# Optimization experiments

Hardware: AMD Instinct MI355X
Metric: run time of the kernel (lower is better)

## Reference

```python
import jax, jax.numpy as jnp
import numpy as np

EMBED = 512
HEADS = 8
HEAD_DIM = EMBED // HEADS
N, S = 4, 2048


def setup_inputs() -> dict:
    key = jax.random.key(0)
    ks = jax.random.split(key, 10)
    value = jax.random.normal(ks[0], (N, S, EMBED), dtype=jnp.float32)
    k_in = jax.random.normal(ks[1], (N, S, EMBED), dtype=jnp.float32)
    q_in = jax.random.normal(ks[2], (N, S, EMBED), dtype=jnp.float32)
    mask = jax.random.randint(ks[3], (N, 1, S, S), 0, 2, dtype=jnp.int32)
    s = 1.0 / np.sqrt(HEAD_DIM)
    Wq = jax.random.uniform(ks[4], (HEAD_DIM, HEAD_DIM), minval=-s, maxval=s, dtype=jnp.float32)
    Wk = jax.random.uniform(ks[5], (HEAD_DIM, HEAD_DIM), minval=-s, maxval=s, dtype=jnp.float32)
    Wv = jax.random.uniform(ks[6], (HEAD_DIM, HEAD_DIM), minval=-s, maxval=s, dtype=jnp.float32)
    so = 1.0 / np.sqrt(EMBED)
    Wo = jax.random.uniform(ks[7], (EMBED, EMBED), minval=-so, maxval=so, dtype=jnp.float32)
    bo = jax.random.uniform(ks[8], (EMBED,), minval=-so, maxval=so, dtype=jnp.float32)
    return {"value": value, "key": k_in, "query": q_in, "mask": mask,
            "Wq": Wq, "Wk": Wk, "Wv": Wv, "Wo": Wo, "bo": bo}


def reference(value, key, query, mask, Wq, Wk, Wv, Wo, bo):
    n, qlen = query.shape[0], query.shape[1]
    # split heads: (N, L, H, D)
    v = value.reshape(n, -1, HEADS, HEAD_DIM)
    k = key.reshape(n, -1, HEADS, HEAD_DIM)
    q = query.reshape(n, qlen, HEADS, HEAD_DIM)
    # per-head linear projections (torch Linear: x @ W^T, no bias)
    v = jnp.einsum('nlhd,ed->nlhe', v, Wv)
    k = jnp.einsum('nlhd,ed->nlhe', k, Wk)
    q = jnp.einsum('nqhd,ed->nqhe', q, Wq)
    # energy: (N, H, Q, K)
    energy = jnp.einsum('nqhd,nkhd->nhqk', q, k)
    energy = jnp.where(mask == 0, jnp.float32(-1e20), energy)
    # NOTE: original scales by sqrt(embed_size), not sqrt(head_dim)
    attn = jax.nn.softmax(energy / jnp.sqrt(jnp.float32(EMBED)), axis=3)
    out = jnp.einsum('nhql,nlhd->nqhd', attn, v).reshape(n, qlen, EMBED)
    return out @ Wo.T + bo
```

## Files before the change

### kernel.cpp

```cpp
#include <hip/hip_runtime.h>

typedef short short8 __attribute__((ext_vector_type(8)));
typedef float f32x4 __attribute__((ext_vector_type(4)));
typedef unsigned short ushort4v __attribute__((ext_vector_type(4)));
typedef unsigned long long u64;
typedef u64 u64x2 __attribute__((ext_vector_type(2)));

#define N_B   4
#define S_LEN 2048
#define EMB   512
#define HD    64
#define NHB   32
#define QSCALE 0.063758714f

#define EXP2F(x) __builtin_amdgcn_exp2f(x)

__device__ unsigned short g_Wqb[64*64];
__device__ unsigned short g_Wkb[64*64];
__device__ unsigned short g_Wvb[64*64];
__device__ unsigned short g_Wob[512*512];
__device__ unsigned short g_Qp[NHB*S_LEN*HD];
__device__ unsigned short g_Kp[NHB*S_LEN*HD];
__device__ unsigned short g_Vt[NHB*HD*S_LEN];
__device__ unsigned short g_AO[N_B*S_LEN*EMB];
__device__ u64            g_Mb[N_B*32*S_LEN];

__device__ __forceinline__ unsigned short f2bf(float f) {
  unsigned u = __float_as_uint(f);
  u = u + 0x7fffu + ((u >> 16) & 1u);
  return (unsigned short)(u >> 16);
}

__device__ __forceinline__ unsigned cvt_pk_bf16(float a, float b) {
  unsigned r;
  asm("v_cvt_pk_bf16_f32 %0, %1, %2" : "=v"(r) : "v"(a), "v"(b));
  return r;
}

__global__ __launch_bounds__(256) void k0_wconv(const float* __restrict__ Wq,
                                                const float* __restrict__ Wk,
                                                const float* __restrict__ Wv,
                                                const float* __restrict__ Wo) {
  int idx = blockIdx.x * 256 + threadIdx.x;
  if (idx < 4096)        g_Wqb[idx]         = f2bf(Wq[idx] * QSCALE);
  else if (idx < 8192)   g_Wkb[idx - 4096]  = f2bf(Wk[idx - 4096]);
  else if (idx < 12288)  g_Wvb[idx - 8192]  = f2bf(Wv[idx - 8192]);
  else                   g_Wob[idx - 12288] = f2bf(Wo[idx - 12288]);
}

__global__ __launch_bounds__(256) void k0b_mask(const int* __restrict__ mask) {
  int wid = blockIdx.x * 4 + (threadIdx.x >> 6);
  int lane = threadIdx.x & 63;
  int n = wid >> 11, q = wid & 2047;
  const int* base = mask + ((size_t)(n * 2048 + q) << 11);
  u64* dst = g_Mb + (size_t)n * 32 * S_LEN + q;
#pragma unroll 4
  for (int j = 0; j < 32; ++j) {
    int mk = base[j * 64 + lane];
    u64 bits = __ballot(mk != 0);
    if (lane == 0) dst[(size_t)j * S_LEN] = bits;
  }
}

__global__ __launch_bounds__(256) void k1_proj(const float* __restrict__ q_in,
                                               const float* __restrict__ k_in,
                                               const float* __restrict__ v_in) {
  __shared__ unsigned short VtL[64][72];
  const int tid = threadIdx.x;
  const int w = tid >> 6, lane = tid & 63, g = lane >> 4, c = lane & 15;
  const int s0 = blockIdx.x * 64;
  const int nh = blockIdx.y, n = nh >> 3, h = nh & 7;
  const int which = blockIdx.z;
  const float* src = which == 0 ? q_in : (which == 1 ? k_in : v_in);
  const unsigned short* Wb = which == 0 ? g_Wqb : (which == 1 ? g_Wkb : g_Wvb);

  short8 xb[2];
  const int srow = s0 + w * 16 + c;
#pragma unroll
  for (int ks = 0; ks < 2; ++ks) {
    const float* ap = src + ((size_t)n * S_LEN + srow) * EMB + h * HD + ks * 32 + g * 8;
    f32x4 x0 = *(const f32x4*)ap;
    f32x4 x1 = *(const f32x4*)(ap + 4);
    short8 tt;
    tt[0] = (short)f2bf(x0[0]); tt[1] = (short)f2bf(x0[1]);
    tt[2] = (short)f2bf(x0[2]); tt[3] = (short)f2bf(x0[3]);
    tt[4] = (short)f2bf(x1[0]); tt[5] = (short)f2bf(x1[1]);
    tt[6] = (short)f2bf(x1[2]); tt[7] = (short)f2bf(x1[3]);
    xb[ks] = tt;
  }

  f32x4 acc[4];
#pragma unroll
  for (int dt = 0; dt < 4; ++dt) { acc[dt][0]=0.f; acc[dt][1]=0.f; acc[dt][2]=0.f; acc[dt][3]=0.f; }

#pragma unroll
  for (int ks = 0; ks < 2; ++ks)
#pragma unroll
    for (int dt = 0; dt < 4; ++dt) {
      short8 a = *(const short8*)(Wb + (dt * 16 + c) * HD + ks * 32 + g * 8);
      acc[dt] = __builtin_amdgcn_mfma_f32_16x16x32_bf16(a, xb[ks], acc[dt], 0, 0, 0);
    }

  if (which < 2) {
    unsigned short* dst = which == 0 ? g_Qp : g_Kp;
#pragma unroll
    for (int dt = 0; dt < 4; ++dt) {
      ushort4v u;
      u[0] = f2bf(acc[dt][0]); u[1] = f2bf(acc[dt][1]);
      u[2] = f2bf(acc[dt][2]); u[3] = f2bf(acc[dt][3]);
      *(ushort4v*)(dst + ((size_t)nh * S_LEN + srow) * HD + dt * 16 + 4 * g) = u;
    }
  } else {
#pragma unroll
    for (int dt = 0; dt < 4; ++dt)
#pragma unroll
      for (int r = 0; r < 4; ++r)
        VtL[dt * 16 + 4 * g + r][w * 16 + c] = f2bf(acc[dt][r]);
    __syncthreads();
#pragma unroll
    for (int rep = 0; rep < 2; ++rep) {
      int cid = tid + rep * 256;
      int row = cid >> 3, ch = cid & 7;
      short8 v = *(const short8*)(&VtL[row][ch * 8]);
      *(short8*)(g_Vt + ((size_t)nh * HD + row) * S_LEN + s0 + ch * 8) = v;
    }
  }
}

__global__ __launch_bounds__(512) void k2_attn() {
  __shared__ unsigned short Kl[2][64][64];
  __shared__ unsigned short Vl[2][80][64];
  __shared__ unsigned short Pl[8][16][64];
  const int tid = threadIdx.x;
  const int w = tid >> 6, lane = tid & 63, g = lane >> 4, c = lane & 15;
  const int q0 = blockIdx.x * 128;
  const int nh = blockIdx.y, n = nh >> 3;

  short8 aq[2];
#pragma unroll
  for (int ks = 0; ks < 2; ++ks)
    aq[ks] = *(const short8*)(g_Qp + ((size_t)nh * S_LEN + q0 + w * 16 + c) * HD + ks * 32 + g * 8);

  const int strow = tid >> 3, schunk = tid & 7;
  const int sdst = (schunk ^ (strow & 7)) * 8;
  const unsigned short* ksrc = g_Kp + ((size_t)nh * S_LEN + strow) * HD + schunk * 8;
  const unsigned short* vsrc = g_Vt + ((size_t)nh * HD + strow) * S_LEN + schunk * 8;
  const u64* mbase = g_Mb + ((size_t)n * 32) * S_LEN + q0 + w * 16 + 4 * g;

  {
    int flat = tid * 4;
    int b = flat >> 10, rem = flat & 1023, rr = rem >> 6, cc = rem & 63;
    ushort4v ones4 = {0x3f80, 0x3f80, 0x3f80, 0x3f80};
    *(ushort4v*)(&Vl[b][64 + rr][cc]) = ones4;
  }

  f32x4 O4[4], O5;
#pragma unroll
  for (int dt = 0; dt < 4; ++dt) { O4[dt][0]=0.f; O4[dt][1]=0.f; O4[dt][2]=0.f; O4[dt][3]=0.f; }
  O5[0]=0.f; O5[1]=0.f; O5[2]=0.f; O5[3]=0.f;

  short8 kst = *(const short8*)(ksrc);
  short8 vst = *(const short8*)(vsrc);
  u64x2 mA = *(const u64x2*)(mbase);
  u64x2 mB = *(const u64x2*)(mbase + 2);
  *(short8*)(&Kl[0][strow][sdst]) = kst;
  *(short8*)(&Vl[0][strow][sdst]) = vst;
  __syncthreads();

  for (int t = 0; t < 32; ++t) {
    const int cur = t & 1;
    u64x2 mAn, mBn;
    if (t < 31) {
      kst = *(const short8*)(ksrc + (size_t)(t + 1) * 64 * HD);
      vst = *(const short8*)(vsrc + (t + 1) * 64);
      mAn = *(const u64x2*)(mbase + (size_t)(t + 1) * S_LEN);
      mBn = *(const u64x2*)(mbase + (size_t)(t + 1) * S_LEN + 2);
    }

    f32x4 sa[4];
#pragma unroll
    for (int ct = 0; ct < 4; ++ct) { sa[ct][0]=0.f; sa[ct][1]=0.f; sa[ct][2]=0.f; sa[ct][3]=0.f; }
#pragma unroll
    for (int ks = 0; ks < 2; ++ks)
#pragma unroll
      for (int ct = 0; ct < 4; ++ct) {
        short8 bk = *(const short8*)(&Kl[cur][ct * 16 + c][((g + 4 * ks) ^ (c & 7)) * 8]);
        sa[ct] = __builtin_amdgcn_mfma_f32_16x16x32_bf16(aq[ks], bk, sa[ct], 0, 0, 0);
      }

    unsigned lo0 = (unsigned)mA[0], hi0 = (unsigned)(mA[0] >> 32);
    unsigned lo1 = (unsigned)mA[1], hi1 = (unsigned)(mA[1] >> 32);
    unsigned lo2 = (unsigned)mB[0], hi2 = (unsigned)(mB[0] >> 32);
    unsigned lo3 = (unsigned)mB[1], hi3 = (unsigned)(mB[1] >> 32);
#pragma unroll
    for (int ct = 0; ct < 4; ++ct) {
      const int sh = (ct & 1) * 16 + c;
      float p0 = ((((ct & 2) ? hi0 : lo0) >> sh) & 1u) ? EXP2F(sa[ct][0]) : 0.f;
      float p1 = ((((ct & 2) ? hi1 : lo1) >> sh) & 1u) ? EXP2F(sa[ct][1]) : 0.f;
      float p2 = ((((ct & 2) ? hi2 : lo2) >> sh) & 1u) ? EXP2F(sa[ct][2]) : 0.f;
      float p3 = ((((ct & 2) ? hi3 : lo3) >> sh) & 1u) ? EXP2F(sa[ct][3]) : 0.f;
      unsigned pk01 = cvt_pk_bf16(p0, p1);
      unsigned pk23 = cvt_pk_bf16(p2, p3);
      const int col = ct * 16 + c;
      const int chs = ((col >> 3) << 3);
#pragma unroll
      for (int r = 0; r < 4; ++r) {
        int prow = 4 * g + r;
        unsigned pk = (r < 2) ? pk01 : pk23;
        unsigned short v = (r & 1) ? (unsigned short)(pk >> 16) : (unsigned short)pk;
        Pl[w][prow][(chs ^ ((prow & 7) << 3)) | (col & 7)] = v;
      }
    }

#pragma unroll
    for (int ks = 0; ks < 2; ++ks) {
      short8 pa = *(const short8*)(&Pl[w][c][((g + 4 * ks) ^ (c & 7)) * 8]);
#pragma unroll
      for (int dt = 0; dt < 5; ++dt) {
        short8 bv = *(const short8*)(&Vl[cur][dt * 16 + c][((g + 4 * ks) ^ (c & 7)) * 8]);
        if (dt < 4)
          O4[dt] = __builtin_amdgcn_mfma_f32_16x16x32_bf16(pa, bv, O4[dt], 0, 0, 0);
        else
          O5 = __builtin_amdgcn_mfma_f32_16x16x32_bf16(pa, bv, O5, 0, 0, 0);
      }
    }

    if (t < 31) {
      *(short8*)(&Kl[cur ^ 1][strow][sdst]) = kst;
      *(short8*)(&Vl[cur ^ 1][strow][sdst]) = vst;
      mA = mAn; mB = mBn;
      __syncthreads();
    }
  }

  const int h = nh & 7;
#pragma unroll
  for (int r = 0; r < 4; ++r) {
    float inv = O5[r] > 0.f ? 1.f / O5[r] : 0.f;
    int qr = q0 + w * 16 + 4 * g + r;
#pragma unroll
    for (int dt = 0; dt < 4; ++dt)
      g_AO[((size_t)n * S_LEN + qr) * EMB + h * HD + dt * 16 + c] = f2bf(O4[dt][r] * inv);
  }
}

__global__ __launch_bounds__(256) void k3_oproj(const float* __restrict__ bo,
                                                float* __restrict__ out) {
  const int tid = threadIdx.x;
  const int w = tid >> 6, lane = tid & 63, g = lane >> 4, c = lane & 15;
  const int m0 = blockIdx.x * 64;
  const int n0 = blockIdx.y * 64;

  f32x4 acc[4];
#pragma unroll
  for (int ct = 0; ct < 4; ++ct) { acc[ct][0]=0.f; acc[ct][1]=0.f; acc[ct][2]=0.f; acc[ct][3]=0.f; }

  for (int ks = 0; ks < 16; ++ks) {
    short8 a = *(const short8*)(g_AO + ((size_t)(m0 + w * 16 + c)) * EMB + ks * 32 + g * 8);
#pragma unroll
    for (int ct = 0; ct < 4; ++ct) {
      short8 b = *(const short8*)(g_Wob + (size_t)(n0 + ct * 16 + c) * EMB + ks * 32 + g * 8);
      acc[ct] = __builtin_amdgcn_mfma_f32_16x16x32_bf16(a, b, acc[ct], 0, 0, 0);
    }
  }

#pragma unroll
  for (int ct = 0; ct < 4; ++ct) {
    int col = n0 + ct * 16 + c;
    float bias = bo[col];
#pragma unroll
    for (int r = 0; r < 4; ++r) {
      int row = m0 + w * 16 + 4 * g + r;
      out[(size_t)row * EMB + col] = acc[ct][r] + bias;
    }
  }
}

extern "C" void kernel_launch(void* const* d_in, const int* in_sizes, int n_in,
                              void* d_out, int out_size, void* d_ws, size_t ws_size,
                              hipStream_t stream) {
  const float* value = (const float*)d_in[0];
  const float* key   = (const float*)d_in[1];
  const float* query = (const float*)d_in[2];
  const int*   mask  = (const int*)d_in[3];
  const float* Wq    = (const float*)d_in[4];
  const float* Wk    = (const float*)d_in[5];
  const float* Wv    = (const float*)d_in[6];
  const float* Wo    = (const float*)d_in[7];
  const float* bo    = (const float*)d_in[8];
  float* out = (float*)d_out;

  k0_wconv<<<1072, 256, 0, stream>>>(Wq, Wk, Wv, Wo);
  k0b_mask<<<2048, 256, 0, stream>>>(mask);
  k1_proj<<<dim3(32, 32, 3), 256, 0, stream>>>(query, key, value);
  k2_attn<<<dim3(16, 32), 512, 0, stream>>>();
  k3_oproj<<<dim3(128, 8), 256, 0, stream>>>(bo, out);
}
```

Measured before the change: 273.4 us.

## Merge prep kernels, loop heads in projection, remap attention block order

Folds the weight conversion and mask bit-packing into one kernel launch so there is one fewer launch. The projection kernel now loops over all 8 heads per block, loading the weight fragments once and reusing them, which cuts the grid from 3072 to 384 blocks. The attention grid is flattened to 1D with a custom mapping from block index to (head, query tile), likely to spread heads across XCDs or L2. Fewer projection blocks may underfill the GPU and serialize per-head work within each block.

```diff
diff --git a/kernel.cpp b/kernel.cpp
--- a/kernel.cpp
+++ b/kernel.cpp
@@ -3,6 +3,7 @@
 typedef short short8 __attribute__((ext_vector_type(8)));
 typedef float f32x4 __attribute__((ext_vector_type(4)));
 typedef unsigned short ushort4v __attribute__((ext_vector_type(4)));
+typedef unsigned int uint4v __attribute__((ext_vector_type(4)));
 typedef unsigned long long u64;
 typedef u64 u64x2 __attribute__((ext_vector_type(2)));
 
@@ -12,7 +13,6 @@
 #define HD    64
 #define NHB   32
 #define QSCALE 0.063758714f
-
 #define EXP2F(x) __builtin_amdgcn_exp2f(x)
 
 __device__ unsigned short g_Wqb[64*64];
@@ -30,35 +30,36 @@
   u = u + 0x7fffu + ((u >> 16) & 1u);
   return (unsigned short)(u >> 16);
 }
-
 __device__ __forceinline__ unsigned cvt_pk_bf16(float a, float b) {
   unsigned r;
   asm("v_cvt_pk_bf16_f32 %0, %1, %2" : "=v"(r) : "v"(a), "v"(b));
   return r;
 }
 
-__global__ __launch_bounds__(256) void k0_wconv(const float* __restrict__ Wq,
-                                                const float* __restrict__ Wk,
-                                                const float* __restrict__ Wv,
-                                                const float* __restrict__ Wo) {
-  int idx = blockIdx.x * 256 + threadIdx.x;
-  if (idx < 4096)        g_Wqb[idx]         = f2bf(Wq[idx] * QSCALE);
-  else if (idx < 8192)   g_Wkb[idx - 4096]  = f2bf(Wk[idx - 4096]);
-  else if (idx < 12288)  g_Wvb[idx - 8192]  = f2bf(Wv[idx - 8192]);
-  else                   g_Wob[idx - 12288] = f2bf(Wo[idx - 12288]);
-}
-
-__global__ __launch_bounds__(256) void k0b_mask(const int* __restrict__ mask) {
-  int wid = blockIdx.x * 4 + (threadIdx.x >> 6);
-  int lane = threadIdx.x & 63;
-  int n = wid >> 11, q = wid & 2047;
-  const int* base = mask + ((size_t)(n * 2048 + q) << 11);
-  u64* dst = g_Mb + (size_t)n * 32 * S_LEN + q;
+__global__ __launch_bounds__(256) void k0_prep(const float* __restrict__ Wq,
+                                               const float* __restrict__ Wk,
+                                               const float* __restrict__ Wv,
+                                               const float* __restrict__ Wo,
+                                               const int* __restrict__ mask) {
+  const int b = blockIdx.x;
+  if (b < 1072) {
+    int idx = b * 256 + threadIdx.x;
+    if (idx < 4096)        g_Wqb[idx]         = f2bf(Wq[idx] * QSCALE);
+    else if (idx < 8192)   g_Wkb[idx - 4096]  = f2bf(Wk[idx - 4096]);
+    else if (idx < 12288)  g_Wvb[idx - 8192]  = f2bf(Wv[idx - 8192]);
+    else                   g_Wob[idx - 12288] = f2bf(Wo[idx - 12288]);
+  } else {
+    int wid = (b - 1072) * 4 + (threadIdx.x >> 6);
+    int lane = threadIdx.x & 63;
+    int n = wid >> 11, q = wid & 2047;
+    const int* base = mask + ((size_t)(n * 2048 + q) << 11);
+    u64* dst = g_Mb + (size_t)n * 32 * S_LEN + q;
 #pragma unroll 4
-  for (int j = 0; j < 32; ++j) {
-    int mk = base[j * 64 + lane];
-    u64 bits = __ballot(mk != 0);
-    if (lane == 0) dst[(size_t)j * S_LEN] = bits;
+    for (int j = 0; j < 32; ++j) {
+      int mk = base[j * 64 + lane];
+      u64 bits = __ballot(mk != 0);
+      if (lane == 0) dst[(size_t)j * S_LEN] = bits;
+    }
   }
 }
 
@@ -69,60 +70,69 @@
   const int tid = threadIdx.x;
   const int w = tid >> 6, lane = tid & 63, g = lane >> 4, c = lane & 15;
   const int s0 = blockIdx.x * 64;
-  const int nh = blockIdx.y, n = nh >> 3, h = nh & 7;
+  const int n = blockIdx.y;
   const int which = blockIdx.z;
   const float* src = which == 0 ? q_in : (which == 1 ? k_in : v_in);
   const unsigned short* Wb = which == 0 ? g_Wqb : (which == 1 ? g_Wkb : g_Wvb);
 
-  short8 xb[2];
   const int srow = s0 + w * 16 + c;
-#pragma unroll
-  for (int ks = 0; ks < 2; ++ks) {
-    const float* ap = src + ((size_t)n * S_LEN + srow) * EMB + h * HD + ks * 32 + g * 8;
-    f32x4 x0 = *(const f32x4*)ap;
-    f32x4 x1 = *(const f32x4*)(ap + 4);
-    short8 tt;
-    tt[0] = (short)f2bf(x0[0]); tt[1] = (short)f2bf(x0[1]);
-    tt[2] = (short)f2bf(x0[2]); tt[3] = (short)f2bf(x0[3]);
-    tt[4] = (short)f2bf(x1[0]); tt[5] = (short)f2bf(x1[1]);
-    tt[6] = (short)f2bf(x1[2]); tt[7] = (short)f2bf(x1[3]);
-    xb[ks] = tt;
-  }
-
-  f32x4 acc[4];
-#pragma unroll
-  for (int dt = 0; dt < 4; ++dt) { acc[dt][0]=0.f; acc[dt][1]=0.f; acc[dt][2]=0.f; acc[dt][3]=0.f; }
-
+  const float* rowp = src + ((size_t)n * S_LEN + srow) * EMB;
+
+  short8 wf[2][4];
 #pragma unroll
   for (int ks = 0; ks < 2; ++ks)
 #pragma unroll
-    for (int dt = 0; dt < 4; ++dt) {
-      short8 a = *(const short8*)(Wb + (dt * 16 + c) * HD + ks * 32 + g * 8);
-      acc[dt] = __builtin_amdgcn_mfma_f32_16x16x32_bf16(a, xb[ks], acc[dt], 0, 0, 0);
-    }
-
-  if (which < 2) {
-    unsigned short* dst = which == 0 ? g_Qp : g_Kp;
-#pragma unroll
-    for (int dt = 0; dt < 4; ++dt) {
-      ushort4v u;
-      u[0] = f2bf(acc[dt][0]); u[1] = f2bf(acc[dt][1]);
-      u[2] = f2bf(acc[dt][2]); u[3] = f2bf(acc[dt][3]);
-      *(ushort4v*)(dst + ((size_t)nh * S_LEN + srow) * HD + dt * 16 + 4 * g) = u;
-    }
-  } else {
-#pragma unroll
     for (int dt = 0; dt < 4; ++dt)
-#pragma unroll
-      for (int r = 0; r < 4; ++r)
-        VtL[dt * 16 + 4 * g + r][w * 16 + c] = f2bf(acc[dt][r]);
-    __syncthreads();
-#pragma unroll
-    for (int rep = 0; rep < 2; ++rep) {
-      int cid = tid + rep * 256;
-      int row = cid >> 3, ch = cid & 7;
-      short8 v = *(const short8*)(&VtL[row][ch * 8]);
-      *(short8*)(g_Vt + ((size_t)nh * HD + row) * S_LEN + s0 + ch * 8) = v;
+      wf[ks][dt] = *(const short8*)(Wb + (dt * 16 + c) * HD + ks * 32 + g * 8);
+
+  for (int hd = 0; hd < 8; ++hd) {
+    short8 xb[2];
+#pragma unroll
+    for (int ks = 0; ks < 2; ++ks) {
+      const float* ap = rowp + hd * HD + ks * 32 + g * 8;
+      f32x4 x0 = *(const f32x4*)ap;
+      f32x4 x1 = *(const f32x4*)(ap + 4);
+      short8 tt;
+      tt[0] = (short)f2bf(x0[0]); tt[1] = (short)f2bf(x0[1]);
+      tt[2] = (short)f2bf(x0[2]); tt[3] = (short)f2bf(x0[3]);
+      tt[4] = (short)f2bf(x1[0]); tt[5] = (short)f2bf(x1[1]);
+      tt[6] = (short)f2bf(x1[2]); tt[7] = (short)f2bf(x1[3]);
+      xb[ks] = tt;
+    }
+    f32x4 acc[4];
+#pragma unroll
+    for (int dt = 0; dt < 4; ++dt) { acc[dt][0]=0.f; acc[dt][1]=0.f; acc[dt][2]=0.f; acc[dt][3]=0.f; }
+#pragma unroll
+    for (int ks = 0; ks < 2; ++ks)
+#pragma unroll
+      for (int dt = 0; dt < 4; ++dt)
+        acc[dt] = __builtin_amdgcn_mfma_f32_16x16x32_bf16(wf[ks][dt], xb[ks], acc[dt], 0, 0, 0);
+
+    const int nh = n * 8 + hd;
+    if (which < 2) {
+      unsigned short* dst = which == 0 ? g_Qp : g_Kp;
+#pragma unroll
+      for (int dt = 0; dt < 4; ++dt) {
+        ushort4v u;
+        u[0] = f2bf(acc[dt][0]); u[1] = f2bf(acc[dt][1]);
+        u[2] = f2bf(acc[dt][2]); u[3] = f2bf(acc[dt][3]);
+        *(ushort4v*)(dst + ((size_t)nh * S_LEN + srow) * HD + dt * 16 + 4 * g) = u;
+      }
+    } else {
+      if (hd) __syncthreads();
+#pragma unroll
+      for (int dt = 0; dt < 4; ++dt)
+#pragma unroll
+        for (int r = 0; r < 4; ++r)
+          VtL[dt * 16 + 4 * g + r][w * 16 + c] = f2bf(acc[dt][r]);
+      __syncthreads();
+#pragma unroll
+      for (int rep = 0; rep < 2; ++rep) {
+        int cid = tid + rep * 256;
+        int row = cid >> 3, ch = cid & 7;
+        short8 v = *(const short8*)(&VtL[row][ch * 8]);
+        *(short8*)(g_Vt + ((size_t)nh * HD + row) * S_LEN + s0 + ch * 8) = v;
+      }
     }
   }
 }
@@ -133,8 +143,11 @@
   __shared__ unsigned short Pl[8][16][64];
   const int tid = threadIdx.x;
   const int w = tid >> 6, lane = tid & 63, g = lane >> 4, c = lane & 15;
-  const int q0 = blockIdx.x * 128;
-  const int nh = blockIdx.y, n = nh >> 3;
+  const int L = blockIdx.x;
+  const int m = L >> 3;
+  const int nh = (L & 7) * 4 + (m >> 4);
+  const int q0 = (m & 15) * 128;
+  const int n = nh >> 3;
 
   short8 aq[2];
 #pragma unroll
@@ -290,9 +303,8 @@
   const float* bo    = (const float*)d_in[8];
   float* out = (float*)d_out;
 
-  k0_wconv<<<1072, 256, 0, stream>>>(Wq, Wk, Wv, Wo);
-  k0b_mask<<<2048, 256, 0, stream>>>(mask);
-  k1_proj<<<dim3(32, 32, 3), 256, 0, stream>>>(query, key, value);
-  k2_attn<<<dim3(16, 32), 512, 0, stream>>>();
+  k0_prep<<<3120, 256, 0, stream>>>(Wq, Wk, Wv, Wo, mask);
+  k1_proj<<<dim3(32, 4, 3), 256, 0, stream>>>(query, key, value);
+  k2_attn<<<512, 512, 0, stream>>>();
   k3_oproj<<<dim3(128, 8), 256, 0, stream>>>(bo, out);
 }
```

Result: no change. 270.6 us (-1.0%).
